# Performance work log

Hardware: AMD Instinct MI355X
Metric: run time of the kernel (lower is better)

Reference implementation:

```python
import jax, jax.numpy as jnp
import numpy as np

B, S, D = 32, 2048, 128


def setup_inputs() -> dict:
    key = jax.random.key(0)
    kq, kk, kv, km = jax.random.split(key, 4)
    queries = jax.random.normal(kq, (B, S, D), dtype=jnp.float32)
    keys = jax.random.normal(kk, (B, S, D), dtype=jnp.float32)
    values = jax.random.normal(kv, (B, S, D), dtype=jnp.float32)
    attention_mask = jax.random.randint(km, (B, S, S), 0, 2, dtype=jnp.int32)
    return {"queries": queries, "keys": keys, "values": values,
            "attention_mask": attention_mask}


def reference(queries, keys, values, attention_mask):
    d = queries.shape[-1]
    # scores: [B, S, S]
    scores = jnp.einsum("bqd,bkd->bqk", queries, keys) / jnp.sqrt(
        jnp.asarray(d, queries.dtype))
    scores = jnp.where(attention_mask == 0, jnp.asarray(-1e6, scores.dtype), scores)
    attn = jax.nn.softmax(scores, axis=-1)
    # dropout prob is 0.0 (eval-equivalent), so no dropout applied
    return jnp.einsum("bqk,bkd->bqd", attn, values)
```

## Files before the change

kernel.cpp:

```cpp
#include <hip/hip_runtime.h>

#define B_ 32
#define S_ 2048
#define D_ 128
#define NT 32
#define QB 256

typedef __bf16 bf16;
typedef unsigned u32;
typedef unsigned long long u64;
typedef __attribute__((ext_vector_type(8))) __bf16 bf16x8;
typedef __attribute__((ext_vector_type(16))) float f32x16;

__device__ __forceinline__ f32x16 mfma32(bf16x8 a, bf16x8 b, f32x16 c) {
  return __builtin_amdgcn_mfma_f32_32x32x16_bf16(a, b, c, 0, 0, 0);
}

__device__ __forceinline__ u32 pk2(bf16 a, bf16 b) {
  unsigned short ua = __builtin_bit_cast(unsigned short, a);
  unsigned short ub = __builtin_bit_cast(unsigned short, b);
  return (u32)ua | ((u32)ub << 16);
}

__global__ __launch_bounds__(256) void vt_prepass(const float* __restrict__ V,
                                                  bf16* __restrict__ vthi,
                                                  bf16* __restrict__ vtlo) {
  const int bid = blockIdx.x;
  const int b = bid >> 5, kt = bid & 31;
  const int kbase = kt * 64;
  const int t = threadIdx.x;
  __shared__ u32 Tpk[128][67];

  {
    const int dc = t & 31, kr0 = t >> 5;
#pragma unroll
    for (int i = 0; i < 8; ++i) {
      const int kr = kr0 + i * 8;
      float4 v = *(const float4*)(V + ((size_t)b * S_ + kbase + kr) * D_ + dc * 4);
      float f[4] = {v.x, v.y, v.z, v.w};
#pragma unroll
      for (int j = 0; j < 4; ++j) {
        bf16 hi = (bf16)f[j];
        bf16 lo = (bf16)(f[j] - (float)hi);
        Tpk[dc * 4 + j][kr] = pk2(hi, lo);
      }
    }
  }
  __syncthreads();
#pragma unroll
  for (int p = 0; p < 4; ++p) {
    const int g = p * 256 + t;
    const int d = g >> 3, c = g & 7;
    const int cs = c ^ (d & 7);
    u32 wv[8];
#pragma unroll
    for (int e = 0; e < 8; ++e) wv[e] = Tpk[d][cs * 8 + e];
    uint4 hi4, lo4;
    u32* hp = (u32*)&hi4;
    u32* lp = (u32*)&lo4;
#pragma unroll
    for (int j = 0; j < 4; ++j) {
      hp[j] = (wv[2 * j] & 0xffffu) | (wv[2 * j + 1] << 16);
      lp[j] = (wv[2 * j] >> 16) | (wv[2 * j + 1] & 0xffff0000u);
    }
    const size_t base = ((size_t)(b * NT + kt) * 128 + d) * 64 + c * 8;
    *(uint4*)(vthi + base) = hi4;
    *(uint4*)(vtlo + base) = lo4;
  }
}

__global__ __launch_bounds__(256) void mask_pack(const int* __restrict__ M,
                                                 u64* __restrict__ bits) {
  const int wv = threadIdx.x >> 6;
  const int lane = threadIdx.x & 63;
  const size_t gw = (size_t)blockIdx.x * 4 + wv;
#pragma unroll 1
  for (int i = 0; i < 16; ++i) {
    const size_t r = gw * 16 + i;
    const int* src = M + r * S_;
    u64* dst = bits + r * NT;
#pragma unroll 1
    for (int c = 0; c < NT; c += 8) {
      u64 bm[8];
#pragma unroll
      for (int j = 0; j < 8; ++j) {
        const int v = src[(c + j) * 64 + lane];
        bm[j] = __ballot(v != 0);
      }
      if (lane == 0) {
#pragma unroll
        for (int j = 0; j < 8; ++j) dst[c + j] = bm[j];
      }
    }
  }
}

__device__ __forceinline__ void k_convert_write(const float4 (&ka)[4], char* kdst,
                                                int t) {
  const int kr = t >> 3;
  float f[16] = {ka[0].x, ka[0].y, ka[0].z, ka[0].w, ka[1].x, ka[1].y,
                 ka[1].z, ka[1].w, ka[2].x, ka[2].y, ka[2].z, ka[2].w,
                 ka[3].x, ka[3].y, ka[3].z, ka[3].w};
  bf16x8 h8[2], l8[2];
#pragma unroll
  for (int q = 0; q < 2; ++q)
#pragma unroll
    for (int e = 0; e < 8; ++e) {
      float v = f[q * 8 + e];
      bf16 hi = (bf16)v;
      h8[q][e] = hi;
      l8[q][e] = (bf16)(v - (float)hi);
    }
  const u32 blk = (u32)(t & 7) * 2, swz = (u32)(kr & 7);
#pragma unroll
  for (int q = 0; q < 2; ++q) {
    const u32 off = (u32)kr * 256 + (((blk + q) ^ swz) * 16);
    *(bf16x8*)(kdst + off) = h8[q];
    *(bf16x8*)(kdst + 16384 + off) = l8[q];
  }
}

__global__ __launch_bounds__(512, 2) void attn_kernel(
    const float* __restrict__ Q, const float* __restrict__ K,
    const u64* __restrict__ MB, const bf16* __restrict__ vthi_g,
    const bf16* __restrict__ vtlo_g, float* __restrict__ Out) {
  extern __shared__ char smem[];
  const int t = threadIdx.x;
  const int w = t >> 6;
  const int i31 = t & 31;
  const int h = (t >> 5) & 1;

  const int bid = blockIdx.x;
  const int b = (bid & 7) * 4 + ((bid >> 3) >> 3);
  const int qbase = ((bid >> 3) & 7) * QB;
  const int qloc = w * 32 + i31;

  const float sc = 0.08838834764831843f * 1.4426950408889634f;
  bf16x8 qh[8], ql[8];
  {
    const float* qsrc = Q + ((size_t)b * S_ + qbase + qloc) * D_;
#pragma unroll
    for (int ds = 0; ds < 8; ++ds) {
      const int d0 = ds * 16 + h * 8;
      float4 a = *(const float4*)(qsrc + d0);
      float4 c = *(const float4*)(qsrc + d0 + 4);
      float f[8] = {a.x, a.y, a.z, a.w, c.x, c.y, c.z, c.w};
#pragma unroll
      for (int e = 0; e < 8; ++e) {
        float v = f[e] * sc;
        bf16 hi = (bf16)v;
        qh[ds][e] = hi;
        ql[ds][e] = (bf16)(v - (float)hi);
      }
    }
  }

  f32x16 acc[4];
#pragma unroll
  for (int dt = 0; dt < 4; ++dt)
#pragma unroll
    for (int e = 0; e < 16; ++e) acc[dt][e] = 0.f;
  float m_run = -3.0e38f, l_run = 0.f;

  const float* kbat = K + (size_t)b * S_ * D_;
  const bf16* vh_b = vthi_g + (size_t)b * NT * 8192;
  const bf16* vl_b = vtlo_g + (size_t)b * NT * 8192;
  const u64* mrow = MB + ((size_t)b * S_ + qbase + qloc) * NT;

  const int kr = t >> 3;
  const int kcol = (t & 7) * 16;

  u64 mcur = mrow[0];
  {
    float4 ka[4];
    const float* ks = kbat + (size_t)kr * D_ + kcol;
#pragma unroll
    for (int j = 0; j < 4; ++j) ka[j] = *(const float4*)(ks + j * 4);
    uint4 vr0 = *(const uint4*)(vh_b + (size_t)t * 8);
    uint4 vr1 = *(const uint4*)(vh_b + (size_t)(512 + t) * 8);
    uint4 vr2 = *(const uint4*)(vl_b + (size_t)t * 8);
    uint4 vr3 = *(const uint4*)(vl_b + (size_t)(512 + t) * 8);
    k_convert_write(ka, smem, t);
    char* vb = smem + 32768;
    *(uint4*)(vb + t * 16) = vr0;
    *(uint4*)(vb + (512 + t) * 16) = vr1;
    *(uint4*)(vb + 16384 + t * 16) = vr2;
    *(uint4*)(vb + 16384 + (512 + t) * 16) = vr3;
  }
  __syncthreads();

  for (int kt = 0; kt < NT; ++kt) {
    const int cb = kt & 1;
    const char* kb = smem + cb * 65536;
    const bool pre = (kt + 1 < NT);
    float4 ka[4];
    uint4 vr0, vr1, vr2, vr3;
    u64 mnxt = 0;
    if (pre) {
      const float* ks = kbat + (size_t)(kt + 1) * 64 * D_ + (size_t)kr * D_ + kcol;
#pragma unroll
      for (int j = 0; j < 4; ++j) ka[j] = *(const float4*)(ks + j * 4);
      const size_t tb = (size_t)(kt + 1) * 8192;
      vr0 = *(const uint4*)(vh_b + tb + (size_t)t * 8);
      vr1 = *(const uint4*)(vh_b + tb + (size_t)(512 + t) * 8);
      vr2 = *(const uint4*)(vl_b + tb + (size_t)t * 8);
      vr3 = *(const uint4*)(vl_b + tb + (size_t)(512 + t) * 8);
      mnxt = mrow[kt + 1];
    }

    f32x16 s[2];
#pragma unroll
    for (int ct = 0; ct < 2; ++ct)
#pragma unroll
      for (int e = 0; e < 16; ++e) s[ct][e] = 0.f;
    __builtin_amdgcn_s_setprio(1);
#pragma unroll
    for (int ct = 0; ct < 2; ++ct) {
      const u32 rowb = (u32)(ct * 32 + i31) * 256;
      const u32 sw = (u32)(i31 & 7) << 4;
#pragma unroll
      for (int ds = 0; ds < 8; ++ds) {
        const u32 off = rowb + (((u32)(ds * 32 + h * 16)) ^ sw);
        bf16x8 kh = *(const bf16x8*)(kb + off);
        bf16x8 kl = *(const bf16x8*)(kb + 16384 + off);
        s[ct] = mfma32(kh, qh[ds], s[ct]);
        s[ct] = mfma32(kl, qh[ds], s[ct]);
        s[ct] = mfma32(kh, ql[ds], s[ct]);
      }
    }
    __builtin_amdgcn_s_setprio(0);

    float mx = -3.0e38f;
#pragma unroll
    for (int ct = 0; ct < 2; ++ct)
#pragma unroll
      for (int r = 0; r < 16; ++r) mx = fmaxf(mx, s[ct][r]);
    mx = fmaxf(mx, __shfl_xor(mx, 32, 64));
    const float m_new = fmaxf(m_run, mx);
    const float alpha = exp2f(m_run - m_new);
    const u32 mw0 = (u32)mcur, mw1 = (u32)(mcur >> 32);
    float rs = 0.f;
#pragma unroll
    for (int ct = 0; ct < 2; ++ct) {
      const u32 mword = ct ? mw1 : mw0;
#pragma unroll
      for (int r = 0; r < 16; ++r) {
        const int pos = (r & 3) + 8 * (r >> 2) + 4 * h;
        float p = exp2f(s[ct][r] - m_new);
        p = ((mword >> pos) & 1u) ? p : 0.f;
        s[ct][r] = p;
        rs += p;
      }
    }
    rs += __shfl_xor(rs, 32, 64);
    l_run = l_run * alpha + rs;
    m_run = m_new;
#pragma unroll
    for (int dt = 0; dt < 4; ++dt) acc[dt] = acc[dt] * alpha;

    const char* vbc = kb + 32768;
    __builtin_amdgcn_s_setprio(1);
#pragma unroll
    for (int ks = 0; ks < 4; ++ks) {
      const int ct = ks >> 1;
      const int a0 = (ks & 1) * 8;
      u32 PKh[4], PKl[4];
#pragma unroll
      for (int y = 0; y < 4; ++y) {
        const float p0 = s[ct][a0 + 2 * y];
        const float p1 = s[ct][a0 + 2 * y + 1];
        bf16 h0 = (bf16)p0, h1 = (bf16)p1;
        PKh[y] = pk2(h0, h1);
        PKl[y] = pk2((bf16)(p0 - (float)h0), (bf16)(p1 - (float)h1));
      }
      const u32 s0h = h ? PKh[0] : PKh[2];
      const u32 s1h = h ? PKh[1] : PKh[3];
      const u32 s0l = h ? PKl[0] : PKl[2];
      const u32 s1l = h ? PKl[1] : PKl[3];
      const u32 r0h = __shfl_xor(s0h, 32, 64);
      const u32 r1h = __shfl_xor(s1h, 32, 64);
      const u32 r0l = __shfl_xor(s0l, 32, 64);
      const u32 r1l = __shfl_xor(s1l, 32, 64);
      uint4 fh, fl;
      fh.x = h ? r0h : PKh[0];
      fh.y = h ? r1h : PKh[1];
      fh.z = h ? PKh[2] : r0h;
      fh.w = h ? PKh[3] : r1h;
      fl.x = h ? r0l : PKl[0];
      fl.y = h ? r1l : PKl[1];
      fl.z = h ? PKl[2] : r0l;
      fl.w = h ? PKl[3] : r1l;
      bf16x8 pah = __builtin_bit_cast(bf16x8, fh);
      bf16x8 pal = __builtin_bit_cast(bf16x8, fl);
#pragma unroll
      for (int dt = 0; dt < 4; ++dt) {
        const u32 d = (u32)(dt * 32 + i31);
        const u32 off = d * 128 + ((((u32)(ks * 2 + h)) ^ (d & 7)) * 16);
        bf16x8 vh = *(const bf16x8*)(vbc + off);
        bf16x8 vl = *(const bf16x8*)(vbc + 16384 + off);
        acc[dt] = mfma32(vh, pah, acc[dt]);
        acc[dt] = mfma32(vh, pal, acc[dt]);
        acc[dt] = mfma32(vl, pah, acc[dt]);
      }
    }
    __builtin_amdgcn_s_setprio(0);

    if (pre) {
      char* kdst = smem + (cb ^ 1) * 65536;
      k_convert_write(ka, kdst, t);
      char* vb = kdst + 32768;
      *(uint4*)(vb + t * 16) = vr0;
      *(uint4*)(vb + (512 + t) * 16) = vr1;
      *(uint4*)(vb + 16384 + t * 16) = vr2;
      *(uint4*)(vb + 16384 + (512 + t) * 16) = vr3;
    }
    __syncthreads();
    mcur = mnxt;
  }

  const float inv_l = 1.0f / l_run;
  float* orow = Out + ((size_t)b * S_ + qbase + qloc) * D_;
#pragma unroll
  for (int dt = 0; dt < 4; ++dt) {
#pragma unroll
    for (int rr = 0; rr < 4; ++rr) {
      float4 o;
      o.x = acc[dt][rr * 4 + 0] * inv_l;
      o.y = acc[dt][rr * 4 + 1] * inv_l;
      o.z = acc[dt][rr * 4 + 2] * inv_l;
      o.w = acc[dt][rr * 4 + 3] * inv_l;
      *(float4*)(orow + dt * 32 + rr * 8 + h * 4) = o;
    }
  }
}

extern "C" void kernel_launch(void* const* d_in, const int* in_sizes, int n_in,
                              void* d_out, int out_size, void* d_ws,
                              size_t ws_size, hipStream_t stream) {
  (void)in_sizes; (void)n_in; (void)out_size; (void)ws_size;
  const float* Q = (const float*)d_in[0];
  const float* K = (const float*)d_in[1];
  const float* V = (const float*)d_in[2];
  const int* M = (const int*)d_in[3];
  float* Out = (float*)d_out;

  const size_t vt_el = (size_t)B_ * S_ * D_;
  bf16* vthi = (bf16*)d_ws;
  bf16* vtlo = vthi + vt_el;
  u64* mbits = (u64*)(vtlo + vt_el);

  static int attr_set = 0;
  if (!attr_set) {
    hipFuncSetAttribute((const void*)attn_kernel,
                        hipFuncAttributeMaxDynamicSharedMemorySize, 131072);
    attr_set = 1;
  }

  vt_prepass<<<dim3(B_ * NT), dim3(256), 0, stream>>>(V, vthi, vtlo);
  mask_pack<<<dim3(1024), dim3(256), 0, stream>>>(M, mbits);
  attn_kernel<<<dim3(256), dim3(512), 131072, stream>>>(Q, K, mbits, vthi, vtlo,
                                                        Out);
}
```

Measured before the change: 957.9 us.

## Fuse mask packing into attention, pre-split K, load tiles via global_load_lds

After: 868.9 us. 1.1x faster.

```diff
diff --git a/kernel.cpp b/kernel.cpp
--- a/kernel.cpp
+++ b/kernel.cpp
@@ -4,7 +4,7 @@
 #define S_ 2048
 #define D_ 128
 #define NT 32
-#define QB 256
+#define QB 128
 
 typedef __bf16 bf16;
 typedef unsigned u32;
@@ -20,6 +20,41 @@
   unsigned short ua = __builtin_bit_cast(unsigned short, a);
   unsigned short ub = __builtin_bit_cast(unsigned short, b);
   return (u32)ua | ((u32)ub << 16);
+}
+
+__device__ __forceinline__ void glds16(const bf16* g, char* l) {
+  __builtin_amdgcn_global_load_lds(
+      (const __attribute__((address_space(1))) void*)g,
+      (__attribute__((address_space(3))) void*)l, 16, 0, 0);
+}
+
+__global__ __launch_bounds__(256) void k_prepass(const float* __restrict__ K,
+                                                 bf16* __restrict__ khi,
+                                                 bf16* __restrict__ klo) {
+  const int bid = blockIdx.x;
+  const int t = threadIdx.x;
+  const int kr = t >> 2;
+  const int cbase = (t & 3) * 4;
+  const float* src = K + (size_t)bid * 8192 + kr * 128;
+  bf16* ho = khi + (size_t)bid * 8192 + kr * 128;
+  bf16* lo = klo + (size_t)bid * 8192 + kr * 128;
+  const int swz = kr & 15;
+#pragma unroll
+  for (int j = 0; j < 4; ++j) {
+    const int c = cbase + j;
+    float4 a = *(const float4*)(src + c * 8);
+    float4 b2 = *(const float4*)(src + c * 8 + 4);
+    float f[8] = {a.x, a.y, a.z, a.w, b2.x, b2.y, b2.z, b2.w};
+    bf16x8 h8, l8;
+#pragma unroll
+    for (int e = 0; e < 8; ++e) {
+      bf16 hi = (bf16)f[e];
+      h8[e] = hi;
+      l8[e] = (bf16)(f[e] - (float)hi);
+    }
+    *(bf16x8*)(ho + (c ^ swz) * 8) = h8;
+    *(bf16x8*)(lo + (c ^ swz) * 8) = l8;
+  }
 }
 
 __global__ __launch_bounds__(256) void vt_prepass(const float* __restrict__ V,
@@ -69,70 +104,22 @@
   }
 }
 
-__global__ __launch_bounds__(256) void mask_pack(const int* __restrict__ M,
-                                                 u64* __restrict__ bits) {
-  const int wv = threadIdx.x >> 6;
-  const int lane = threadIdx.x & 63;
-  const size_t gw = (size_t)blockIdx.x * 4 + wv;
-#pragma unroll 1
-  for (int i = 0; i < 16; ++i) {
-    const size_t r = gw * 16 + i;
-    const int* src = M + r * S_;
-    u64* dst = bits + r * NT;
-#pragma unroll 1
-    for (int c = 0; c < NT; c += 8) {
-      u64 bm[8];
-#pragma unroll
-      for (int j = 0; j < 8; ++j) {
-        const int v = src[(c + j) * 64 + lane];
-        bm[j] = __ballot(v != 0);
-      }
-      if (lane == 0) {
-#pragma unroll
-        for (int j = 0; j < 8; ++j) dst[c + j] = bm[j];
-      }
-    }
-  }
-}
-
-__device__ __forceinline__ void k_convert_write(const float4 (&ka)[4], char* kdst,
-                                                int t) {
-  const int kr = t >> 3;
-  float f[16] = {ka[0].x, ka[0].y, ka[0].z, ka[0].w, ka[1].x, ka[1].y,
-                 ka[1].z, ka[1].w, ka[2].x, ka[2].y, ka[2].z, ka[2].w,
-                 ka[3].x, ka[3].y, ka[3].z, ka[3].w};
-  bf16x8 h8[2], l8[2];
-#pragma unroll
-  for (int q = 0; q < 2; ++q)
-#pragma unroll
-    for (int e = 0; e < 8; ++e) {
-      float v = f[q * 8 + e];
-      bf16 hi = (bf16)v;
-      h8[q][e] = hi;
-      l8[q][e] = (bf16)(v - (float)hi);
-    }
-  const u32 blk = (u32)(t & 7) * 2, swz = (u32)(kr & 7);
-#pragma unroll
-  for (int q = 0; q < 2; ++q) {
-    const u32 off = (u32)kr * 256 + (((blk + q) ^ swz) * 16);
-    *(bf16x8*)(kdst + off) = h8[q];
-    *(bf16x8*)(kdst + 16384 + off) = l8[q];
-  }
-}
-
-__global__ __launch_bounds__(512, 2) void attn_kernel(
-    const float* __restrict__ Q, const float* __restrict__ K,
-    const u64* __restrict__ MB, const bf16* __restrict__ vthi_g,
-    const bf16* __restrict__ vtlo_g, float* __restrict__ Out) {
+__global__ __launch_bounds__(256, 2) void attn_kernel(
+    const float* __restrict__ Q, const int* __restrict__ M,
+    const bf16* __restrict__ khi_g, const bf16* __restrict__ klo_g,
+    const bf16* __restrict__ vthi_g, const bf16* __restrict__ vtlo_g,
+    float* __restrict__ Out) {
   extern __shared__ char smem[];
   const int t = threadIdx.x;
   const int w = t >> 6;
+  const int lane = t & 63;
   const int i31 = t & 31;
   const int h = (t >> 5) & 1;
 
   const int bid = blockIdx.x;
-  const int b = (bid & 7) * 4 + ((bid >> 3) >> 3);
-  const int qbase = ((bid >> 3) & 7) * QB;
+  const int idx = bid >> 3;
+  const int b = (bid & 7) * 4 + (idx >> 4);
+  const int qbase = (idx & 15) * QB;
   const int qloc = w * 32 + i31;
 
   const float sc = 0.08838834764831843f * 1.4426950408889634f;
@@ -162,50 +149,33 @@
     for (int e = 0; e < 16; ++e) acc[dt][e] = 0.f;
   float m_run = -3.0e38f, l_run = 0.f;
 
-  const float* kbat = K + (size_t)b * S_ * D_;
-  const bf16* vh_b = vthi_g + (size_t)b * NT * 8192;
-  const bf16* vl_b = vtlo_g + (size_t)b * NT * 8192;
-  const u64* mrow = MB + ((size_t)b * S_ + qbase + qloc) * NT;
-
-  const int kr = t >> 3;
-  const int kcol = (t & 7) * 16;
-
-  u64 mcur = mrow[0];
-  {
-    float4 ka[4];
-    const float* ks = kbat + (size_t)kr * D_ + kcol;
-#pragma unroll
-    for (int j = 0; j < 4; ++j) ka[j] = *(const float4*)(ks + j * 4);
-    uint4 vr0 = *(const uint4*)(vh_b + (size_t)t * 8);
-    uint4 vr1 = *(const uint4*)(vh_b + (size_t)(512 + t) * 8);
-    uint4 vr2 = *(const uint4*)(vl_b + (size_t)t * 8);
-    uint4 vr3 = *(const uint4*)(vl_b + (size_t)(512 + t) * 8);
-    k_convert_write(ka, smem, t);
-    char* vb = smem + 32768;
-    *(uint4*)(vb + t * 16) = vr0;
-    *(uint4*)(vb + (512 + t) * 16) = vr1;
-    *(uint4*)(vb + 16384 + t * 16) = vr2;
-    *(uint4*)(vb + 16384 + (512 + t) * 16) = vr3;
-  }
+  const bf16* g0 = (w & 2) ? vthi_g : khi_g;
+  const bf16* g1 = (w & 2) ? vtlo_g : klo_g;
+  const bf16* gsel = (w & 1) ? g1 : g0;
+  const size_t tstride = 8192;
+  const bf16* gsrc0 = gsel + (size_t)(b * NT) * tstride + lane * 8;
+  char* ldst = smem + w * 16384;
+
+  const int* mptr = M + ((size_t)b * S_ + qbase + w * 32) * S_ + lane;
+
+#pragma unroll
+  for (int i = 0; i < 16; ++i) glds16(gsrc0 + i * 512, ldst + i * 1024);
+  int mv[32];
+#pragma unroll
+  for (int r = 0; r < 32; ++r) mv[r] = mptr[r * S_];
   __syncthreads();
 
   for (int kt = 0; kt < NT; ++kt) {
-    const int cb = kt & 1;
-    const char* kb = smem + cb * 65536;
-    const bool pre = (kt + 1 < NT);
-    float4 ka[4];
-    uint4 vr0, vr1, vr2, vr3;
-    u64 mnxt = 0;
-    if (pre) {
-      const float* ks = kbat + (size_t)(kt + 1) * 64 * D_ + (size_t)kr * D_ + kcol;
-#pragma unroll
-      for (int j = 0; j < 4; ++j) ka[j] = *(const float4*)(ks + j * 4);
-      const size_t tb = (size_t)(kt + 1) * 8192;
-      vr0 = *(const uint4*)(vh_b + tb + (size_t)t * 8);
-      vr1 = *(const uint4*)(vh_b + tb + (size_t)(512 + t) * 8);
-      vr2 = *(const uint4*)(vl_b + tb + (size_t)t * 8);
-      vr3 = *(const uint4*)(vl_b + tb + (size_t)(512 + t) * 8);
-      mnxt = mrow[kt + 1];
+    u64 mc = 0;
+#pragma unroll
+    for (int r = 0; r < 32; ++r) {
+      const u64 bal = __ballot(mv[r] != 0);
+      if (i31 == r) mc = bal;
+    }
+    {
+      const int knb = ((kt + 1 < NT) ? kt + 1 : kt) * 64;
+#pragma unroll
+      for (int r = 0; r < 32; ++r) mv[r] = mptr[r * S_ + knb];
     }
 
     f32x16 s[2];
@@ -217,12 +187,12 @@
 #pragma unroll
     for (int ct = 0; ct < 2; ++ct) {
       const u32 rowb = (u32)(ct * 32 + i31) * 256;
-      const u32 sw = (u32)(i31 & 7) << 4;
+      const u32 sw = (u32)(i31 & 15);
 #pragma unroll
       for (int ds = 0; ds < 8; ++ds) {
-        const u32 off = rowb + (((u32)(ds * 32 + h * 16)) ^ sw);
-        bf16x8 kh = *(const bf16x8*)(kb + off);
-        bf16x8 kl = *(const bf16x8*)(kb + 16384 + off);
+        const u32 off = rowb + (((u32)(ds * 2 + h) ^ sw) * 16);
+        bf16x8 kh = *(const bf16x8*)(smem + off);
+        bf16x8 kl = *(const bf16x8*)(smem + 16384 + off);
         s[ct] = mfma32(kh, qh[ds], s[ct]);
         s[ct] = mfma32(kl, qh[ds], s[ct]);
         s[ct] = mfma32(kh, ql[ds], s[ct]);
@@ -238,7 +208,7 @@
     mx = fmaxf(mx, __shfl_xor(mx, 32, 64));
     const float m_new = fmaxf(m_run, mx);
     const float alpha = exp2f(m_run - m_new);
-    const u32 mw0 = (u32)mcur, mw1 = (u32)(mcur >> 32);
+    const u32 mw0 = (u32)mc, mw1 = (u32)(mc >> 32);
     float rs = 0.f;
 #pragma unroll
     for (int ct = 0; ct < 2; ++ct) {
@@ -258,7 +228,6 @@
 #pragma unroll
     for (int dt = 0; dt < 4; ++dt) acc[dt] = acc[dt] * alpha;
 
-    const char* vbc = kb + 32768;
     __builtin_amdgcn_s_setprio(1);
 #pragma unroll
     for (int ks = 0; ks < 4; ++ks) {
@@ -296,8 +265,8 @@
       for (int dt = 0; dt < 4; ++dt) {
         const u32 d = (u32)(dt * 32 + i31);
         const u32 off = d * 128 + ((((u32)(ks * 2 + h)) ^ (d & 7)) * 16);
-        bf16x8 vh = *(const bf16x8*)(vbc + off);
-        bf16x8 vl = *(const bf16x8*)(vbc + 16384 + off);
+        bf16x8 vh = *(const bf16x8*)(smem + 32768 + off);
+        bf16x8 vl = *(const bf16x8*)(smem + 49152 + off);
         acc[dt] = mfma32(vh, pah, acc[dt]);
         acc[dt] = mfma32(vh, pal, acc[dt]);
         acc[dt] = mfma32(vl, pah, acc[dt]);
@@ -305,17 +274,13 @@
     }
     __builtin_amdgcn_s_setprio(0);
 
-    if (pre) {
-      char* kdst = smem + (cb ^ 1) * 65536;
-      k_convert_write(ka, kdst, t);
-      char* vb = kdst + 32768;
-      *(uint4*)(vb + t * 16) = vr0;
-      *(uint4*)(vb + (512 + t) * 16) = vr1;
-      *(uint4*)(vb + 16384 + t * 16) = vr2;
-      *(uint4*)(vb + 16384 + (512 + t) * 16) = vr3;
-    }
     __syncthreads();
-    mcur = mnxt;
+    if (kt + 1 < NT) {
+      const bf16* gsrc = gsrc0 + (size_t)(kt + 1) * tstride;
+#pragma unroll
+      for (int i = 0; i < 16; ++i) glds16(gsrc + i * 512, ldst + i * 1024);
+    }
+    __syncthreads();
   }
 
   const float inv_l = 1.0f / l_run;
@@ -344,20 +309,21 @@
   const int* M = (const int*)d_in[3];
   float* Out = (float*)d_out;
 
-  const size_t vt_el = (size_t)B_ * S_ * D_;
-  bf16* vthi = (bf16*)d_ws;
-  bf16* vtlo = vthi + vt_el;
-  u64* mbits = (u64*)(vtlo + vt_el);
+  const size_t el = (size_t)B_ * S_ * D_;
+  bf16* khi = (bf16*)d_ws;
+  bf16* klo = khi + el;
+  bf16* vthi = klo + el;
+  bf16* vtlo = vthi + el;
 
   static int attr_set = 0;
   if (!attr_set) {
     hipFuncSetAttribute((const void*)attn_kernel,
-                        hipFuncAttributeMaxDynamicSharedMemorySize, 131072);
+                        hipFuncAttributeMaxDynamicSharedMemorySize, 65536);
     attr_set = 1;
   }
 
+  k_prepass<<<dim3(B_ * NT), dim3(256), 0, stream>>>(K, khi, klo);
   vt_prepass<<<dim3(B_ * NT), dim3(256), 0, stream>>>(V, vthi, vtlo);
-  mask_pack<<<dim3(1024), dim3(256), 0, stream>>>(M, mbits);
-  attn_kernel<<<dim3(256), dim3(512), 131072, stream>>>(Q, K, mbits, vthi, vtlo,
-                                                        Out);
-}
+  attn_kernel<<<dim3(512), dim3(256), 65536, stream>>>(Q, M, khi, klo, vthi,
+                                                       vtlo, Out);
+}
```
